# Optimization experiments

Hardware: AMD Instinct MI355X
Metric: run time of the kernel (lower is better)

Reference implementation:

```python
import jax, jax.numpy as jnp
import numpy as np

N = 50000
E = 800000
IN_DIM = 128
HID = 64
OUT_DIM = 1
NEG_SLOPE = 0.2
EPS = 1e-16


def _glorot(key, shape):
    fan = shape[-1] + (shape[0] if len(shape) > 1 else shape[-1])
    lim = jnp.sqrt(6.0 / fan)
    return jax.random.uniform(key, shape, jnp.float32, -lim, lim)


def setup_inputs() -> dict:
    key = jax.random.key(0)
    ks = jax.random.split(key, 12)
    x = jax.random.normal(ks[0], (N, IN_DIM), jnp.float32)
    edge_index = jax.random.randint(ks[1], (2, E), 0, N, jnp.int64)
    # GATConv layer 1: in=128, out=64, heads=4, concat=True
    W1 = _glorot(ks[2], (4 * HID, IN_DIM))
    att_src1 = _glorot(ks[3], (4, HID))
    att_dst1 = _glorot(ks[4], (4, HID))
    b1 = jnp.zeros((4 * HID,), jnp.float32)
    # GATConv layer 2: in=256, out=64, heads=1, concat=True
    W2 = _glorot(ks[5], (HID, 4 * HID))
    att_src2 = _glorot(ks[6], (1, HID))
    att_dst2 = _glorot(ks[7], (1, HID))
    b2 = jnp.zeros((HID,), jnp.float32)
    # final Linear(hidden, 1)
    fc_w = _glorot(ks[8], (OUT_DIM, HID))
    fc_b = jnp.zeros((OUT_DIM,), jnp.float32)
    return {"x": x, "edge_index": edge_index, "W1": W1, "att_src1": att_src1,
            "att_dst1": att_dst1, "b1": b1, "W2": W2, "att_src2": att_src2,
            "att_dst2": att_dst2, "b2": b2, "fc_w": fc_w, "fc_b": fc_b}


def _gat_layer(x, src, dst, W, att_src, att_dst, bias, heads, out_ch):
    n = x.shape[0]
    xt = (x @ W.T).reshape(n, heads, out_ch)          # [N, H, C]
    a_src = jnp.sum(xt * att_src[None], axis=-1)      # [N, H]
    a_dst = jnp.sum(xt * att_dst[None], axis=-1)      # [N, H]
    e = a_src[src] + a_dst[dst]                       # [E', H]
    e = jnp.where(e > 0, e, NEG_SLOPE * e)            # LeakyReLU(0.2)
    # segment softmax over incoming edges of each dst node
    m = jax.ops.segment_max(e, dst, num_segments=n)
    e = jnp.exp(e - m[dst])
    s = jax.ops.segment_sum(e, dst, num_segments=n)
    alpha = e / (s[dst] + EPS)                        # [E', H]
    msg = xt[src] * alpha[:, :, None]                 # [E', H, C]
    out = jax.ops.segment_sum(msg, dst, num_segments=n)
    return out.reshape(n, heads * out_ch) + bias


def reference(x, edge_index, W1, att_src1, att_dst1, b1,
              W2, att_src2, att_dst2, b2, fc_w, fc_b):
    n = x.shape[0]
    # PyG GATConv default: add self-loops
    loops = jnp.arange(n, dtype=edge_index.dtype)
    src = jnp.concatenate([edge_index[0], loops])
    dst = jnp.concatenate([edge_index[1], loops])
    h = jax.nn.relu(_gat_layer(x, src, dst, W1, att_src1, att_dst1, b1, 4, HID))
    h = jax.nn.relu(_gat_layer(h, src, dst, W2, att_src2, att_dst2, b2, 1, HID))
    logits = h @ fc_w.T + fc_b                        # [N, 1]
    return jax.nn.sigmoid(logits).squeeze()
```

## Files before the change

kernel.cpp:

```cpp
#include <hip/hip_runtime.h>
#include <hip/hip_bf16.h>

#define NN 50000
#define EE 800000
#define ET (NN + EE)
#define SG ((NN + 255) / 256)
#define GB1 ((NN + 63) / 64)

typedef __attribute__((ext_vector_type(8))) short short8;
typedef __attribute__((ext_vector_type(4))) float f32x4;

__device__ __forceinline__ float bf2f(unsigned short u) {
    union { unsigned int i; float f; } v; v.i = ((unsigned int)u) << 16; return v.f;
}
__device__ __forceinline__ unsigned short f2bf(float f) {
    __hip_bfloat16 h = __float2bfloat16(f);
    return *reinterpret_cast<unsigned short*>(&h);
}
__device__ __forceinline__ float lrelu(float e) { return e > 0.f ? e : 0.2f * e; }


__global__ void k_hist(const int* __restrict__ dst, int* __restrict__ cnt) {
    int i = blockIdx.x * blockDim.x + threadIdx.x;
    if (i < EE) atomicAdd(&cnt[dst[i]], 1);
}

__global__ __launch_bounds__(256) void k_scan1(const int* __restrict__ cnt,
                                               int* __restrict__ tmp, int* __restrict__ bsum) {
    int b = blockIdx.x, t = threadIdx.x, i = b * 256 + t;
    int lane = t & 63, w = t >> 6;
    int v = (i < NN) ? cnt[i] : 0;
    int s = v;
    #pragma unroll
    for (int off = 1; off < 64; off <<= 1) {
        int u = __shfl_up(s, off);
        if (lane >= off) s += u;
    }
    __shared__ int ws[4];
    if (lane == 63) ws[w] = s;
    __syncthreads();
    if (t == 0) {
        int a = 0;
        #pragma unroll
        for (int k = 0; k < 4; k++) { int x = ws[k]; ws[k] = a; a += x; }
        bsum[b] = a;
    }
    __syncthreads();
    s += ws[w];
    if (i < NN) tmp[i] = s;
}

__global__ __launch_bounds__(256) void k_scan2(const int* __restrict__ bsum, int* __restrict__ boff) {
    int t = threadIdx.x, lane = t & 63, w = t >> 6;
    int v = (t < SG) ? bsum[t] : 0;
    int s = v;
    #pragma unroll
    for (int off = 1; off < 64; off <<= 1) {
        int u = __shfl_up(s, off);
        if (lane >= off) s += u;
    }
    __shared__ int ws[4];
    if (lane == 63) ws[w] = s;
    __syncthreads();
    if (t == 0) {
        int a = 0;
        #pragma unroll
        for (int k = 0; k < 4; k++) { int x = ws[k]; ws[k] = a; a += x; }
    }
    __syncthreads();
    s += ws[w];
    if (t < SG) boff[t] = s - v;
}

__global__ void k_scan3_prep(const int* __restrict__ tmp, const int* __restrict__ boff,
                             int* __restrict__ rowptr, int* __restrict__ writeptr,
                             int* __restrict__ csr) {
    int i = blockIdx.x * blockDim.x + threadIdx.x;
    if (i == 0) rowptr[0] = 0;
    if (i < NN) {
        int base = boff[i >> 8];
        int incl = tmp[i] + base + i + 1;
        rowptr[i + 1] = incl;
        int excl = ((i & 255) ? tmp[i - 1] + base : base) + i;
        csr[excl] = i;
        writeptr[i] = excl + 1;
    }
}

template<int K, int N, int NH, bool A_BF16>
__device__ __forceinline__ void gemm_body(
    int bid, const void* __restrict__ Aptr, const float* __restrict__ W,
    const float* __restrict__ atts, const float* __restrict__ attd,
    unsigned short* __restrict__ C, float* __restrict__ as_, float* __restrict__ ad_,
    int M)
{
    constexpr int KU  = K / 8;
    constexpr int KUH = KU / 2;
    constexpr int KC  = K / 32;
    constexpr int NW  = N / 4;
    constexpr int NI  = NW / 16;
    constexpr int ABYTES = 64 * KU * 16;
    constexpr int BBYTES = N * KUH * 16;
    constexpr int SMEM = ABYTES + BBYTES + (NH == 1 ? 2048 : 0);
    __shared__ char smem[SMEM];
    char* Ash = smem;
    char* Bsh = smem + ABYTES;
    unsigned short* Csh = (unsigned short*)smem;
    float* scsh = (float*)(smem + ABYTES + BBYTES);

    int t = threadIdx.x;
    int lane = t & 63, w = t >> 6;
    int colL = lane & 15, quad = lane >> 4;
    int m0 = bid * 64;

    {
        constexpr int CNT = 64 * KU / 256;
        #pragma unroll
        for (int i = 0; i < CNT; i++) {
            int v = t + 256 * i;
            int m = v / KU, u = v % KU;
            int gr = m0 + m; if (gr >= M) gr = M - 1;
            short8 val;
            if (A_BF16) {
                val = *(const short8*)((const unsigned short*)Aptr + (size_t)gr * K + u * 8);
            } else {
                const float* Af = (const float*)Aptr;
                float4 lo = *(const float4*)(Af + (size_t)gr * K + u * 8);
                float4 hi = *(const float4*)(Af + (size_t)gr * K + u * 8 + 4);
                val[0] = (short)f2bf(lo.x); val[1] = (short)f2bf(lo.y);
                val[2] = (short)f2bf(lo.z); val[3] = (short)f2bf(lo.w);
                val[4] = (short)f2bf(hi.x); val[5] = (short)f2bf(hi.y);
                val[6] = (short)f2bf(hi.z); val[7] = (short)f2bf(hi.w);
            }
            *(short8*)(Ash + ((size_t)m * KU + (u ^ (m & 7))) * 16) = val;
        }
    }

    f32x4 acc[4][NI];
    #pragma unroll
    for (int mi = 0; mi < 4; mi++)
        #pragma unroll
        for (int ni = 0; ni < NI; ni++) acc[mi][ni] = (f32x4){0.f, 0.f, 0.f, 0.f};

    #pragma unroll
    for (int kh = 0; kh < 2; kh++) {
        __syncthreads();
        {
            constexpr int CNT = N * KUH / 256;
            #pragma unroll
            for (int i = 0; i < CNT; i++) {
                int v = t + 256 * i;
                int n = v / KUH, uu = v % KUH;
                int u = kh * KUH + uu;
                float4 lo = *(const float4*)(W + (size_t)n * K + u * 8);
                float4 hi = *(const float4*)(W + (size_t)n * K + u * 8 + 4);
                short8 val;
                val[0] = (short)f2bf(lo.x); val[1] = (short)f2bf(lo.y);
                val[2] = (short)f2bf(lo.z); val[3] = (short)f2bf(lo.w);
                val[4] = (short)f2bf(hi.x); val[5] = (short)f2bf(hi.y);
                val[6] = (short)f2bf(hi.z); val[7] = (short)f2bf(hi.w);
                *(short8*)(Bsh + ((size_t)n * KUH + (uu ^ (n & 7))) * 16) = val;
            }
        }
        __syncthreads();
        #pragma unroll
        for (int kcl = 0; kcl < KC / 2; kcl++) {
            int uA = (kh * (KC / 2) + kcl) * 4 + quad;
            int uB = kcl * 4 + quad;
            short8 bf[NI];
            #pragma unroll
            for (int ni = 0; ni < NI; ni++) {
                int n = w * NW + ni * 16 + colL;
                bf[ni] = *(const short8*)(Bsh + ((size_t)n * KUH + (uB ^ (n & 7))) * 16);
            }
            #pragma unroll
            for (int mi = 0; mi < 4; mi++) {
                int m = mi * 16 + colL;
                short8 af = *(const short8*)(Ash + ((size_t)m * KU + (uA ^ (m & 7))) * 16);
                #pragma unroll
                for (int ni = 0; ni < NI; ni++)
                    acc[mi][ni] = __builtin_amdgcn_mfma_f32_16x16x32_bf16(af, bf[ni], acc[mi][ni], 0, 0, 0);
            }
        }
    }
    __syncthreads();

    float asv[NI], adv[NI];
    #pragma unroll
    for (int ni = 0; ni < NI; ni++) {
        int na = (NH == 4) ? (w * 64 + ni * 16 + colL) : (w * 16 + colL);
        asv[ni] = atts[na];
        adv[ni] = attd[na];
    }
    #pragma unroll
    for (int mi = 0; mi < 4; mi++) {
        float ps[4] = {0.f, 0.f, 0.f, 0.f}, pd[4] = {0.f, 0.f, 0.f, 0.f};
        #pragma unroll
        for (int ni = 0; ni < NI; ni++)
            #pragma unroll
            for (int r = 0; r < 4; r++) {
                ps[r] += acc[mi][ni][r] * asv[ni];
                pd[r] += acc[mi][ni][r] * adv[ni];
            }
        #pragma unroll
        for (int off = 1; off < 16; off <<= 1)
            #pragma unroll
            for (int r = 0; r < 4; r++) {
                ps[r] += __shfl_xor(ps[r], off);
                pd[r] += __shfl_xor(pd[r], off);
            }
        if (colL == 0) {
            #pragma unroll
            for (int r = 0; r < 4; r++) {
                int rloc = mi * 16 + quad * 4 + r;
                if (NH == 4) {
                    int row = m0 + rloc;
                    if (row < M) {
                        as_[(size_t)row * 4 + w] = ps[r];
                        ad_[(size_t)row * 4 + w] = pd[r];
                    }
                } else {
                    scsh[(w * 64 + rloc) * 2 + 0] = ps[r];
                    scsh[(w * 64 + rloc) * 2 + 1] = pd[r];
                }
            }
        }
    }

    #pragma unroll
    for (int mi = 0; mi < 4; mi++)
        #pragma unroll
        for (int ni = 0; ni < NI; ni++)
            #pragma unroll
            for (int r = 0; r < 4; r++)
                Csh[(size_t)(mi * 16 + quad * 4 + r) * (N + 8) + w * NW + ni * 16 + colL] =
                    f2bf(acc[mi][ni][r]);
    __syncthreads();

    {
        constexpr int CNT = 64 * (N / 8) / 256;
        #pragma unroll
        for (int i = 0; i < CNT; i++) {
            int v = t + 256 * i;
            int m = v / (N / 8), u = v % (N / 8);
            int row = m0 + m;
            if (row < M)
                *(short8*)(C + (size_t)row * N + u * 8) =
                    *(const short8*)(Csh + (size_t)m * (N + 8) + u * 8);
        }
    }
    if (NH == 1 && t < 64) {
        int row = m0 + t;
        if (row < M) {
            float s = 0.f, d = 0.f;
            #pragma unroll
            for (int ww = 0; ww < 4; ww++) {
                s += scsh[(ww * 64 + t) * 2 + 0];
                d += scsh[(ww * 64 + t) * 2 + 1];
            }
            as_[row] = s;
            ad_[row] = d;
        }
    }
}

template<int K, int N, int NH, bool A_BF16>
__global__ __launch_bounds__(256) void k_gemm_mfma(
    const void* __restrict__ Aptr, const float* __restrict__ W,
    const float* __restrict__ atts, const float* __restrict__ attd,
    unsigned short* __restrict__ C, float* __restrict__ as_, float* __restrict__ ad_,
    int M)
{
    gemm_body<K, N, NH, A_BF16>(blockIdx.x, Aptr, W, atts, attd, C, as_, ad_, M);
}

__global__ __launch_bounds__(256) void k_gemm1_scatter(
    const void* __restrict__ Aptr, const float* __restrict__ W,
    const float* __restrict__ atts, const float* __restrict__ attd,
    unsigned short* __restrict__ C, float* __restrict__ as_, float* __restrict__ ad_,
    int M,
    const int* __restrict__ src, const int* __restrict__ dst,
    int* __restrict__ writeptr, int* __restrict__ csr)
{
    int bid = blockIdx.x;
    int g = bid / 5, r = bid % 5;
    if (r == 0 && g < GB1) {
        gemm_body<128, 256, 4, false>(g, Aptr, W, atts, attd, C, as_, ad_, M);
    } else {
        int ng = (r == 0) ? g : g + 1;
        if (ng > GB1) ng = GB1;
        int sb = bid - ng;
        int i = sb * 256 + threadIdx.x;
        if (i < EE) {
            int pos = atomicAdd(&writeptr[dst[i]], 1);
            csr[pos] = src[i];
        }
    }
}

__global__ __launch_bounds__(256) void k_l1_agg(
    const unsigned short* __restrict__ xt1, const float* __restrict__ as1,
    const float* __restrict__ ad1, const int* __restrict__ rowptr,
    const int* __restrict__ csr, const float* __restrict__ b1,
    unsigned short* __restrict__ h1)
{
    int t = threadIdx.x;
    int lane = t & 63, w = t >> 6;
    int n = blockIdx.x * 4 + w;
    int beg = rowptr[n], deg = rowptr[n + 1] - beg;
    int half = lane >> 5, c = lane & 31, h = c >> 3;
    float adh = ad1[n * 4 + h];

    float acc[8] = {0.f, 0.f, 0.f, 0.f, 0.f, 0.f, 0.f, 0.f};
    float esum = 0.f;
    int j = 0;
    for (; j + 4 <= deg; j += 4) {
        int p = beg + j + half * 2;
        int s0 = csr[p], s1 = csr[p + 1];
        float e0 = __expf(lrelu(as1[s0 * 4 + h] + adh));
        float e1 = __expf(lrelu(as1[s1 * 4 + h] + adh));
        short8 r0 = *(const short8*)(xt1 + (size_t)s0 * 256 + c * 8);
        short8 r1 = *(const short8*)(xt1 + (size_t)s1 * 256 + c * 8);
        esum += e0 + e1;
        #pragma unroll
        for (int k = 0; k < 8; k++)
            acc[k] += bf2f((unsigned short)r0[k]) * e0 + bf2f((unsigned short)r1[k]) * e1;
    }
    for (; j < deg; j += 2) {
        int jj = j + half;
        if (jj < deg) {
            int p = beg + jj;
            int s = csr[p];
            float e = __expf(lrelu(as1[s * 4 + h] + adh));
            short8 r = *(const short8*)(xt1 + (size_t)s * 256 + c * 8);
            esum += e;
            #pragma unroll
            for (int k = 0; k < 8; k++) acc[k] += bf2f((unsigned short)r[k]) * e;
        }
    }
    #pragma unroll
    for (int k = 0; k < 8; k++) acc[k] += __shfl_xor(acc[k], 32);
    esum += __shfl_xor(esum, 32);
    if (half == 0) {
        float rs = 1.f / (esum + 1e-16f);
        float4 bl = *(const float4*)(b1 + c * 8);
        float4 bh = *(const float4*)(b1 + c * 8 + 4);
        float bb[8] = {bl.x, bl.y, bl.z, bl.w, bh.x, bh.y, bh.z, bh.w};
        short8 o;
        #pragma unroll
        for (int k = 0; k < 8; k++)
            o[k] = (short)f2bf(fmaxf(acc[k] * rs + bb[k], 0.f));
        *(short8*)(h1 + (size_t)n * 256 + c * 8) = o;
    }
}

__global__ __launch_bounds__(256) void k_l2_agg(
    const unsigned short* __restrict__ xt2, const float* __restrict__ as2,
    const float* __restrict__ ad2, const int* __restrict__ rowptr,
    const int* __restrict__ csr, const float* __restrict__ b2,
    const float* __restrict__ fcw, const float* __restrict__ fcb,
    float* __restrict__ out)
{
    int t = threadIdx.x;
    int lane = t & 63, w = t >> 6;
    int n = blockIdx.x * 4 + w;
    int beg = rowptr[n], deg = rowptr[n + 1] - beg;
    int half = lane >> 5, c = lane & 31;
    float adv = ad2[n];

    float a0 = 0.f, a1 = 0.f, esum = 0.f;
    int j = 0;
    for (; j + 4 <= deg; j += 4) {
        int p = beg + j + half * 2;
        int s0 = csr[p], s1 = csr[p + 1];
        float e0 = __expf(lrelu(as2[s0] + adv));
        float e1 = __expf(lrelu(as2[s1] + adv));
        unsigned int r0 = *(const unsigned int*)(xt2 + (size_t)s0 * 64 + c * 2);
        unsigned int r1 = *(const unsigned int*)(xt2 + (size_t)s1 * 64 + c * 2);
        esum += e0 + e1;
        a0 += bf2f(r0 & 0xffff) * e0 + bf2f(r1 & 0xffff) * e1;
        a1 += bf2f(r0 >> 16) * e0 + bf2f(r1 >> 16) * e1;
    }
    for (; j < deg; j += 2) {
        int jj = j + half;
        if (jj < deg) {
            int p = beg + jj;
            int s = csr[p];
            float e = __expf(lrelu(as2[s] + adv));
            unsigned int r = *(const unsigned int*)(xt2 + (size_t)s * 64 + c * 2);
            esum += e;
            a0 += bf2f(r & 0xffff) * e;
            a1 += bf2f(r >> 16) * e;
        }
    }
    a0 += __shfl_xor(a0, 32);
    a1 += __shfl_xor(a1, 32);
    esum += __shfl_xor(esum, 32);
    if (half == 0) {
        float rs = 1.f / (esum + 1e-16f);
        float o0 = fmaxf(a0 * rs + b2[c * 2], 0.f);
        float o1 = fmaxf(a1 * rs + b2[c * 2 + 1], 0.f);
        float z = o0 * fcw[c * 2] + o1 * fcw[c * 2 + 1];
        #pragma unroll
        for (int off = 16; off; off >>= 1) z += __shfl_xor(z, off);
        if (c == 0) out[n] = 1.f / (1.f + __expf(-(z + fcb[0])));
    }
}


extern "C" void kernel_launch(void* const* d_in, const int* in_sizes, int n_in,
                              void* d_out, int out_size, void* d_ws, size_t ws_size,
                              hipStream_t stream) {
    const float* x    = (const float*)d_in[0];
    const int*   ei   = (const int*)d_in[1];
    const float* W1   = (const float*)d_in[2];
    const float* as1w = (const float*)d_in[3];
    const float* ad1w = (const float*)d_in[4];
    const float* b1   = (const float*)d_in[5];
    const float* W2   = (const float*)d_in[6];
    const float* as2w = (const float*)d_in[7];
    const float* ad2w = (const float*)d_in[8];
    const float* b2   = (const float*)d_in[9];
    const float* fcw  = (const float*)d_in[10];
    const float* fcb  = (const float*)d_in[11];
    float* out = (float*)d_out;

    const int* src = ei;
    const int* dst = ei + EE;

    char* base = (char*)d_ws;
    size_t off = 0;
    auto alloc = [&](size_t bytes) -> void* {
        void* p = base + off;
        off = (off + bytes + 255) & ~(size_t)255;
        return p;
    };
    int*   rowptr   = (int*)alloc((NN + 1) * sizeof(int));
    int*   cnt      = (int*)alloc(NN * sizeof(int));
    int*   tmp      = (int*)alloc(NN * sizeof(int));
    int*   bsum     = (int*)alloc(SG * sizeof(int));
    int*   boff     = (int*)alloc(SG * sizeof(int));
    int*   writeptr = (int*)alloc(NN * sizeof(int));
    int*   csr      = (int*)alloc(ET * sizeof(int));
    unsigned short* xt1 = (unsigned short*)alloc((size_t)NN * 256 * sizeof(unsigned short));
    unsigned short* h1  = (unsigned short*)alloc((size_t)NN * 256 * sizeof(unsigned short));
    float* as1      = (float*)alloc(NN * 4 * sizeof(float));
    float* ad1      = (float*)alloc(NN * 4 * sizeof(float));
    float* as2      = (float*)alloc(NN * sizeof(float));
    float* ad2      = (float*)alloc(NN * sizeof(float));
    unsigned short* xt2 = xt1;

    hipMemsetAsync(cnt, 0, NN * sizeof(int), stream);
    k_hist<<<(EE + 255) / 256, 256, 0, stream>>>(dst, cnt);
    k_scan1<<<SG, 256, 0, stream>>>(cnt, tmp, bsum);
    k_scan2<<<1, 256, 0, stream>>>(bsum, boff);
    k_scan3_prep<<<SG, 256, 0, stream>>>(tmp, boff, rowptr, writeptr, csr);

    int fused_blocks = GB1 + (EE + 255) / 256;
    k_gemm1_scatter<<<fused_blocks, 256, 0, stream>>>(
        x, W1, as1w, ad1w, xt1, as1, ad1, NN, src, dst, writeptr, csr);

    k_l1_agg<<<(NN + 3) / 4, 256, 0, stream>>>(xt1, as1, ad1, rowptr, csr, b1, h1);
    k_gemm_mfma<256, 64, 1, true><<<GB1, 256, 0, stream>>>(
        h1, W2, as2w, ad2w, xt2, as2, ad2, NN);
    k_l2_agg<<<(NN + 3) / 4, 256, 0, stream>>>(xt2, as2, ad2, rowptr, csr, b2, fcw, fcb, out);
}
```

Baseline: 289.9 us.

## Fuse layer-1 aggregation with layer-2 GEMM through shared memory

The layer-1 aggregation now writes each 64-row tile of h1 directly into swizzled shared memory, and the same block runs the layer-2 MFMA GEMM plus the attention-score reductions on it. This removes the h1 global round trip (write and reread of N×256 bf16) and one kernel launch. In exchange, the block count drops from N/4 to N/64, and each wave processes 16 nodes serially. That may reduce the number of gathers in flight and the latency hiding for the irregular aggregation, and the large LDS footprint limits occupancy.

```diff
diff --git a/kernel.cpp b/kernel.cpp
--- a/kernel.cpp
+++ b/kernel.cpp
@@ -264,16 +264,6 @@
     }
 }
 
-template<int K, int N, int NH, bool A_BF16>
-__global__ __launch_bounds__(256) void k_gemm_mfma(
-    const void* __restrict__ Aptr, const float* __restrict__ W,
-    const float* __restrict__ atts, const float* __restrict__ attd,
-    unsigned short* __restrict__ C, float* __restrict__ as_, float* __restrict__ ad_,
-    int M)
-{
-    gemm_body<K, N, NH, A_BF16>(blockIdx.x, Aptr, W, atts, attd, C, as_, ad_, M);
-}
-
 __global__ __launch_bounds__(256) void k_gemm1_scatter(
     const void* __restrict__ Aptr, const float* __restrict__ W,
     const float* __restrict__ atts, const float* __restrict__ attd,
@@ -298,59 +288,183 @@
     }
 }
 
-__global__ __launch_bounds__(256) void k_l1_agg(
+__global__ __launch_bounds__(256) void k_l1_gemm2(
     const unsigned short* __restrict__ xt1, const float* __restrict__ as1,
     const float* __restrict__ ad1, const int* __restrict__ rowptr,
     const int* __restrict__ csr, const float* __restrict__ b1,
-    unsigned short* __restrict__ h1)
+    const float* __restrict__ W2, const float* __restrict__ atts,
+    const float* __restrict__ attd, unsigned short* __restrict__ xt2,
+    float* __restrict__ as2, float* __restrict__ ad2)
 {
+    constexpr int K = 256, N = 64;
+    constexpr int KU = K / 8;
+    constexpr int KUH = KU / 2;
+    constexpr int KC = K / 32;
+    constexpr int NW = N / 4;
+    constexpr int ABYTES = 64 * KU * 16;
+    constexpr int BBYTES = N * KUH * 16;
+    __shared__ char smem[ABYTES + BBYTES + 2048];
+    char* Ash = smem;
+    char* Bsh = smem + ABYTES;
+    unsigned short* Csh = (unsigned short*)smem;
+    float* scsh = (float*)(smem + ABYTES + BBYTES);
+
     int t = threadIdx.x;
     int lane = t & 63, w = t >> 6;
-    int n = blockIdx.x * 4 + w;
-    int beg = rowptr[n], deg = rowptr[n + 1] - beg;
+    int m0 = blockIdx.x * 64;
+
     int half = lane >> 5, c = lane & 31, h = c >> 3;
-    float adh = ad1[n * 4 + h];
-
-    float acc[8] = {0.f, 0.f, 0.f, 0.f, 0.f, 0.f, 0.f, 0.f};
-    float esum = 0.f;
-    int j = 0;
-    for (; j + 4 <= deg; j += 4) {
-        int p = beg + j + half * 2;
-        int s0 = csr[p], s1 = csr[p + 1];
-        float e0 = __expf(lrelu(as1[s0 * 4 + h] + adh));
-        float e1 = __expf(lrelu(as1[s1 * 4 + h] + adh));
-        short8 r0 = *(const short8*)(xt1 + (size_t)s0 * 256 + c * 8);
-        short8 r1 = *(const short8*)(xt1 + (size_t)s1 * 256 + c * 8);
-        esum += e0 + e1;
-        #pragma unroll
-        for (int k = 0; k < 8; k++)
-            acc[k] += bf2f((unsigned short)r0[k]) * e0 + bf2f((unsigned short)r1[k]) * e1;
-    }
-    for (; j < deg; j += 2) {
-        int jj = j + half;
-        if (jj < deg) {
-            int p = beg + jj;
-            int s = csr[p];
-            float e = __expf(lrelu(as1[s * 4 + h] + adh));
-            short8 r = *(const short8*)(xt1 + (size_t)s * 256 + c * 8);
-            esum += e;
-            #pragma unroll
-            for (int k = 0; k < 8; k++) acc[k] += bf2f((unsigned short)r[k]) * e;
-        }
-    }
-    #pragma unroll
-    for (int k = 0; k < 8; k++) acc[k] += __shfl_xor(acc[k], 32);
-    esum += __shfl_xor(esum, 32);
-    if (half == 0) {
-        float rs = 1.f / (esum + 1e-16f);
-        float4 bl = *(const float4*)(b1 + c * 8);
-        float4 bh = *(const float4*)(b1 + c * 8 + 4);
-        float bb[8] = {bl.x, bl.y, bl.z, bl.w, bh.x, bh.y, bh.z, bh.w};
-        short8 o;
-        #pragma unroll
-        for (int k = 0; k < 8; k++)
-            o[k] = (short)f2bf(fmaxf(acc[k] * rs + bb[k], 0.f));
-        *(short8*)(h1 + (size_t)n * 256 + c * 8) = o;
+    float4 bl = *(const float4*)(b1 + c * 8);
+    float4 bh = *(const float4*)(b1 + c * 8 + 4);
+    float bb[8] = {bl.x, bl.y, bl.z, bl.w, bh.x, bh.y, bh.z, bh.w};
+
+    for (int rep = 0; rep < 16; rep++) {
+        int m = w * 16 + rep;
+        int n = m0 + m;
+        float acc[8] = {0.f, 0.f, 0.f, 0.f, 0.f, 0.f, 0.f, 0.f};
+        float esum = 0.f;
+        if (n < NN) {
+            int beg = rowptr[n], deg = rowptr[n + 1] - beg;
+            float adh = ad1[n * 4 + h];
+            int j = 0;
+            for (; j + 4 <= deg; j += 4) {
+                int p = beg + j + half * 2;
+                int s0 = csr[p], s1 = csr[p + 1];
+                float e0 = __expf(lrelu(as1[s0 * 4 + h] + adh));
+                float e1 = __expf(lrelu(as1[s1 * 4 + h] + adh));
+                short8 r0 = *(const short8*)(xt1 + (size_t)s0 * 256 + c * 8);
+                short8 r1 = *(const short8*)(xt1 + (size_t)s1 * 256 + c * 8);
+                esum += e0 + e1;
+                #pragma unroll
+                for (int k = 0; k < 8; k++)
+                    acc[k] += bf2f((unsigned short)r0[k]) * e0 + bf2f((unsigned short)r1[k]) * e1;
+            }
+            for (; j < deg; j += 2) {
+                int jj = j + half;
+                if (jj < deg) {
+                    int p = beg + jj;
+                    int s = csr[p];
+                    float e = __expf(lrelu(as1[s * 4 + h] + adh));
+                    short8 r = *(const short8*)(xt1 + (size_t)s * 256 + c * 8);
+                    esum += e;
+                    #pragma unroll
+                    for (int k = 0; k < 8; k++) acc[k] += bf2f((unsigned short)r[k]) * e;
+                }
+            }
+        }
+        #pragma unroll
+        for (int k = 0; k < 8; k++) acc[k] += __shfl_xor(acc[k], 32);
+        esum += __shfl_xor(esum, 32);
+        if (half == 0) {
+            float rs = 1.f / (esum + 1e-16f);
+            short8 o;
+            #pragma unroll
+            for (int k = 0; k < 8; k++)
+                o[k] = (short)f2bf((n < NN) ? fmaxf(acc[k] * rs + bb[k], 0.f) : 0.f);
+            *(short8*)(Ash + ((size_t)m * KU + (c ^ (m & 7))) * 16) = o;
+        }
+    }
+
+    int colL = lane & 15, quad = lane >> 4;
+    f32x4 acc2[4];
+    #pragma unroll
+    for (int mi = 0; mi < 4; mi++) acc2[mi] = (f32x4){0.f, 0.f, 0.f, 0.f};
+
+    #pragma unroll
+    for (int kh = 0; kh < 2; kh++) {
+        __syncthreads();
+        {
+            constexpr int CNT = N * KUH / 256;
+            #pragma unroll
+            for (int i = 0; i < CNT; i++) {
+                int v = t + 256 * i;
+                int nn = v / KUH, uu = v % KUH;
+                int u = kh * KUH + uu;
+                float4 lo = *(const float4*)(W2 + (size_t)nn * K + u * 8);
+                float4 hi = *(const float4*)(W2 + (size_t)nn * K + u * 8 + 4);
+                short8 val;
+                val[0] = (short)f2bf(lo.x); val[1] = (short)f2bf(lo.y);
+                val[2] = (short)f2bf(lo.z); val[3] = (short)f2bf(lo.w);
+                val[4] = (short)f2bf(hi.x); val[5] = (short)f2bf(hi.y);
+                val[6] = (short)f2bf(hi.z); val[7] = (short)f2bf(hi.w);
+                *(short8*)(Bsh + ((size_t)nn * KUH + (uu ^ (nn & 7))) * 16) = val;
+            }
+        }
+        __syncthreads();
+        #pragma unroll
+        for (int kcl = 0; kcl < KC / 2; kcl++) {
+            int uA = (kh * (KC / 2) + kcl) * 4 + quad;
+            int uB = kcl * 4 + quad;
+            int nn = w * NW + colL;
+            short8 bf = *(const short8*)(Bsh + ((size_t)nn * KUH + (uB ^ (nn & 7))) * 16);
+            #pragma unroll
+            for (int mi = 0; mi < 4; mi++) {
+                int m = mi * 16 + colL;
+                short8 af = *(const short8*)(Ash + ((size_t)m * KU + (uA ^ (m & 7))) * 16);
+                acc2[mi] = __builtin_amdgcn_mfma_f32_16x16x32_bf16(af, bf, acc2[mi], 0, 0, 0);
+            }
+        }
+    }
+    __syncthreads();
+
+    float asv = atts[w * NW + colL];
+    float adv = attd[w * NW + colL];
+    #pragma unroll
+    for (int mi = 0; mi < 4; mi++) {
+        float ps[4], pd[4];
+        #pragma unroll
+        for (int r = 0; r < 4; r++) {
+            ps[r] = acc2[mi][r] * asv;
+            pd[r] = acc2[mi][r] * adv;
+        }
+        #pragma unroll
+        for (int off = 1; off < 16; off <<= 1)
+            #pragma unroll
+            for (int r = 0; r < 4; r++) {
+                ps[r] += __shfl_xor(ps[r], off);
+                pd[r] += __shfl_xor(pd[r], off);
+            }
+        if (colL == 0) {
+            #pragma unroll
+            for (int r = 0; r < 4; r++) {
+                int rloc = mi * 16 + quad * 4 + r;
+                scsh[(w * 64 + rloc) * 2 + 0] = ps[r];
+                scsh[(w * 64 + rloc) * 2 + 1] = pd[r];
+            }
+        }
+    }
+
+    #pragma unroll
+    for (int mi = 0; mi < 4; mi++)
+        #pragma unroll
+        for (int r = 0; r < 4; r++)
+            Csh[(size_t)(mi * 16 + quad * 4 + r) * (N + 8) + w * NW + colL] =
+                f2bf(acc2[mi][r]);
+    __syncthreads();
+    {
+        constexpr int CNT = 64 * (N / 8) / 256;
+        #pragma unroll
+        for (int i = 0; i < CNT; i++) {
+            int v = t + 256 * i;
+            int m = v / (N / 8), u = v % (N / 8);
+            int row = m0 + m;
+            if (row < NN)
+                *(short8*)(xt2 + (size_t)row * N + u * 8) =
+                    *(const short8*)(Csh + (size_t)m * (N + 8) + u * 8);
+        }
+    }
+    if (t < 64) {
+        int row = m0 + t;
+        if (row < NN) {
+            float s = 0.f, d = 0.f;
+            #pragma unroll
+            for (int ww = 0; ww < 4; ww++) {
+                s += scsh[(ww * 64 + t) * 2 + 0];
+                d += scsh[(ww * 64 + t) * 2 + 1];
+            }
+            as2[row] = s;
+            ad2[row] = d;
+        }
     }
 }
 
@@ -443,12 +557,11 @@
     int*   writeptr = (int*)alloc(NN * sizeof(int));
     int*   csr      = (int*)alloc(ET * sizeof(int));
     unsigned short* xt1 = (unsigned short*)alloc((size_t)NN * 256 * sizeof(unsigned short));
-    unsigned short* h1  = (unsigned short*)alloc((size_t)NN * 256 * sizeof(unsigned short));
+    unsigned short* xt2 = (unsigned short*)alloc((size_t)NN * 64 * sizeof(unsigned short));
     float* as1      = (float*)alloc(NN * 4 * sizeof(float));
     float* ad1      = (float*)alloc(NN * 4 * sizeof(float));
     float* as2      = (float*)alloc(NN * sizeof(float));
     float* ad2      = (float*)alloc(NN * sizeof(float));
-    unsigned short* xt2 = xt1;
 
     hipMemsetAsync(cnt, 0, NN * sizeof(int), stream);
     k_hist<<<(EE + 255) / 256, 256, 0, stream>>>(dst, cnt);
@@ -460,8 +573,8 @@
     k_gemm1_scatter<<<fused_blocks, 256, 0, stream>>>(
         x, W1, as1w, ad1w, xt1, as1, ad1, NN, src, dst, writeptr, csr);
 
-    k_l1_agg<<<(NN + 3) / 4, 256, 0, stream>>>(xt1, as1, ad1, rowptr, csr, b1, h1);
-    k_gemm_mfma<256, 64, 1, true><<<GB1, 256, 0, stream>>>(
-        h1, W2, as2w, ad2w, xt2, as2, ad2, NN);
-    k_l2_agg<<<(NN + 3) / 4, 256, 0, stream>>>(xt2, as2, ad2, rowptr, csr, b2, fcw, fcb, out);
-}
+    k_l1_gemm2<<<GB1, 256, 0, stream>>>(
+        xt1, as1, ad1, rowptr, csr, b1, W2, as2w, ad2w, xt2, as2, ad2);
+
+    k_l2_agg<<<NN / 4, 256, 0, stream>>>(xt2, as2, ad2, rowptr, csr, b2, fcw, fcb, out);
+}
```

New measurement: 351.8 us. 1.21x slower.
